# Kernel tuning notes

Hardware: AMD Instinct MI355X
Metric: run time of the kernel (lower is better)

Reference implementation:

```python
import jax, jax.numpy as jnp
import numpy as np

EPS = 1e-5  # torch LayerNorm default

def layer_norm(x, g, b):
    m = jnp.mean(x)
    v = jnp.mean((x - m) ** 2)  # biased variance, as in torch LayerNorm
    return (x - m) * jax.lax.rsqrt(v + EPS) * g + b

def setup_inputs() -> dict:
    key = jax.random.key(0)
    ks = jax.random.split(key, 8)
    sz_I, sz_H1, sz_H2, sz_O = 2048, 4096, 4096, 1024
    def w(k, out_d, in_d):
        return jax.random.normal(k, (out_d, in_d), dtype=jnp.float32) / np.sqrt(in_d)
    return {
        "input_raw": jax.random.normal(ks[0], (sz_I,), dtype=jnp.float32),
        "h2_prev": jax.random.normal(ks[1], (sz_H2,), dtype=jnp.float32),
        "W_I_H1": w(ks[2], sz_H1, sz_I),
        "W_H2_H1": w(ks[3], sz_H1, sz_H2),
        "W_H1_H2": w(ks[4], sz_H2, sz_H1),
        "W_H1_O": w(ks[5], sz_O, sz_H1),
        "W_H2_O": w(ks[6], sz_O, sz_H2),
        "g_H1": jnp.ones((sz_H1,), jnp.float32), "b_H1": jnp.zeros((sz_H1,), jnp.float32),
        "g_H2": jnp.ones((sz_H2,), jnp.float32), "b_H2": jnp.zeros((sz_H2,), jnp.float32),
        "g_O": jnp.ones((sz_O,), jnp.float32), "b_O": jnp.zeros((sz_O,), jnp.float32),
    }

def reference(input_raw, h2_prev, W_I_H1, W_H2_H1, W_H1_H2, W_H1_O, W_H2_O,
              g_H1, b_H1, g_H2, b_H2, g_O, b_O):
    act = jnp.tanh
    # message: out_act(in_act(LN_target(W @ x))); with tanh/identity composed = tanh once
    def msg(W, x, g, b):
        return act(layer_norm(W @ x, g, b))
    i_out = input_raw                                   # I layer output
    h1 = msg(W_I_H1, i_out, g_H1, b_H1) + msg(W_H2_H1, h2_prev, g_H1, b_H1)
    h2 = msg(W_H1_H2, h1, g_H2, b_H2)
    o_acc = msg(W_H1_O, h1, g_O, b_O) + msg(W_H2_O, h2, g_O, b_O)
    # final output-layer activation: out_act(LN_O(acc))
    o_final = act(layer_norm(o_acc, g_O, b_O))
    return o_final
```

## Files before the change

kernel.cpp:

```cpp
#include <hip/hip_runtime.h>

#define LN_EPS 1e-5f

__device__ __forceinline__ float wave_sum(float v) {
    #pragma unroll
    for (int o = 32; o; o >>= 1) v += __shfl_down(v, o);
    return v;
}

__device__ __forceinline__ float block_sum_1024(float v, float* sh) {
    int lane = threadIdx.x & 63, w = threadIdx.x >> 6;
    v = wave_sum(v);
    if (lane == 0) sh[w] = v;
    __syncthreads();
    if (w == 0) {
        float s = (lane < 16) ? sh[lane] : 0.f;
        #pragma unroll
        for (int o = 8; o; o >>= 1) s += __shfl_down(s, o);
        if (lane == 0) sh[0] = s;
    }
    __syncthreads();
    float r = sh[0];
    __syncthreads();
    return r;
}

__global__ __launch_bounds__(256) void k1(
        const float* __restrict__ W_I_H1, const float* __restrict__ x_in,
        const float* __restrict__ W_H2_H1, const float* __restrict__ h2_prev,
        float* __restrict__ t1, float* __restrict__ t2,
        float2* __restrict__ p1, float2* __restrict__ p2) {
    extern __shared__ float xs[];
    __shared__ float shy[4];
    const float* W; const float* x; float* y; float2* p; int C; int blk;
    if ((int)blockIdx.x < 1024) {
        W = W_I_H1;  x = x_in;    y = t1; p = p1; C = 2048; blk = blockIdx.x;
    } else {
        W = W_H2_H1; x = h2_prev; y = t2; p = p2; C = 4096; blk = blockIdx.x - 1024;
    }
    int n4 = C >> 2;
    float4* xs4 = (float4*)xs;
    for (int i = threadIdx.x; i < n4; i += 256)
        xs4[i] = ((const float4*)x)[i];
    __syncthreads();

    int wave = threadIdx.x >> 6, lane = threadIdx.x & 63;
    int row = blk * 4 + wave;
    const float4* Wr = (const float4*)(W + (size_t)row * C);
    float acc = 0.f;
    #pragma unroll 4
    for (int i = lane; i < n4; i += 64) {
        float4 w = Wr[i], v = xs4[i];
        acc += w.x * v.x + w.y * v.y + w.z * v.z + w.w * v.w;
    }
    acc = wave_sum(acc);
    if (lane == 0) { y[row] = acc; shy[wave] = acc; }
    __syncthreads();
    if (threadIdx.x == 0) {
        float s = 0.f, q = 0.f;
        #pragma unroll
        for (int i = 0; i < 4; i++) { float v = shy[i]; s += v; q += v * v; }
        p[blk] = make_float2(s, q);
    }
}

__global__ __launch_bounds__(1024) void ln2_add(
        const float* __restrict__ t1, const float* __restrict__ t2,
        const float2* __restrict__ p1, const float2* __restrict__ p2,
        const float* __restrict__ g, const float* __restrict__ b,
        float* __restrict__ h1) {
    __shared__ float sh[16];
    int tid = threadIdx.x;
    float2 a = p1[tid], c = p2[tid];
    float s1 = block_sum_1024(a.x, sh), q1 = block_sum_1024(a.y, sh);
    float s2 = block_sum_1024(c.x, sh), q2 = block_sum_1024(c.y, sh);
    const float invN = 1.f / 4096.f;
    float m1 = s1 * invN, r1 = rsqrtf(fmaxf(q1 * invN - m1 * m1, 0.f) + LN_EPS);
    float m2 = s2 * invN, r2 = rsqrtf(fmaxf(q2 * invN - m2 * m2, 0.f) + LN_EPS);

    float4 av = ((const float4*)t1)[tid], cv = ((const float4*)t2)[tid];
    float4 gv = ((const float4*)g)[tid], bv = ((const float4*)b)[tid];
    float4 o;
    o.x = tanhf((av.x - m1) * r1 * gv.x + bv.x) + tanhf((cv.x - m2) * r2 * gv.x + bv.x);
    o.y = tanhf((av.y - m1) * r1 * gv.y + bv.y) + tanhf((cv.y - m2) * r2 * gv.y + bv.y);
    o.z = tanhf((av.z - m1) * r1 * gv.z + bv.z) + tanhf((cv.z - m2) * r2 * gv.z + bv.z);
    o.w = tanhf((av.w - m1) * r1 * gv.w + bv.w) + tanhf((cv.w - m2) * r2 * gv.w + bv.w);
    ((float4*)h1)[tid] = o;
}

__global__ __launch_bounds__(256) void k2(
        const float* __restrict__ h1,
        const float* __restrict__ W_H1_H2, const float* __restrict__ W_H1_O,
        float* __restrict__ t3, float* __restrict__ t4,
        float2* __restrict__ p3, float2* __restrict__ p4) {
    extern __shared__ float xs[];
    __shared__ float shy[4];
    float4* xs4 = (float4*)xs;
    for (int i = threadIdx.x; i < 1024; i += 256)
        xs4[i] = ((const float4*)h1)[i];
    __syncthreads();

    const float* W; float* y; float2* p; int blk;
    if ((int)blockIdx.x < 1024) { W = W_H1_H2; y = t3; p = p3; blk = blockIdx.x; }
    else                        { W = W_H1_O;  y = t4; p = p4; blk = blockIdx.x - 1024; }
    int wave = threadIdx.x >> 6, lane = threadIdx.x & 63;
    int row = blk * 4 + wave;
    const float4* Wr = (const float4*)(W + (size_t)row * 4096);
    float acc = 0.f;
    #pragma unroll 4
    for (int i = lane; i < 1024; i += 64) {
        float4 w = Wr[i], v = xs4[i];
        acc += w.x * v.x + w.y * v.y + w.z * v.z + w.w * v.w;
    }
    acc = wave_sum(acc);
    if (lane == 0) { y[row] = acc; shy[wave] = acc; }
    __syncthreads();
    if (threadIdx.x == 0) {
        float s = 0.f, q = 0.f;
        #pragma unroll
        for (int i = 0; i < 4; i++) { float v = shy[i]; s += v; q += v * v; }
        p[blk] = make_float2(s, q);
    }
}

__global__ __launch_bounds__(1024) void ln_tanh(
        const float* __restrict__ t3, const float2* __restrict__ p3,
        const float* __restrict__ g, const float* __restrict__ b,
        float* __restrict__ h2) {
    __shared__ float sh[16];
    int tid = threadIdx.x;
    float2 a = p3[tid];
    float s3 = block_sum_1024(a.x, sh), q3 = block_sum_1024(a.y, sh);
    const float invN = 1.f / 4096.f;
    float m3 = s3 * invN, r3 = rsqrtf(fmaxf(q3 * invN - m3 * m3, 0.f) + LN_EPS);

    float4 av = ((const float4*)t3)[tid];
    float4 gv = ((const float4*)g)[tid], bv = ((const float4*)b)[tid];
    float4 o;
    o.x = tanhf((av.x - m3) * r3 * gv.x + bv.x);
    o.y = tanhf((av.y - m3) * r3 * gv.y + bv.y);
    o.z = tanhf((av.z - m3) * r3 * gv.z + bv.z);
    o.w = tanhf((av.w - m3) * r3 * gv.w + bv.w);
    ((float4*)h2)[tid] = o;
}

__global__ __launch_bounds__(256) void k3(
        const float* __restrict__ h2, const float* __restrict__ W_H2_O,
        float* __restrict__ t5, float2* __restrict__ p5) {
    extern __shared__ float xs[];
    __shared__ float shp[4];
    float4* xs4 = (float4*)xs;
    for (int i = threadIdx.x; i < 1024; i += 256)
        xs4[i] = ((const float4*)h2)[i];
    __syncthreads();

    int wave = threadIdx.x >> 6, lane = threadIdx.x & 63;
    int row  = blockIdx.x * 2 + (wave >> 1);
    int half = wave & 1;
    const float4* Wr = (const float4*)(W_H2_O + (size_t)row * 4096);
    float acc = 0.f;
    int i0 = half * 512 + lane;
    #pragma unroll 8
    for (int k = 0; k < 8; k++) {
        int i = i0 + k * 64;
        float4 w = Wr[i], v = xs4[i];
        acc += w.x * v.x + w.y * v.y + w.z * v.z + w.w * v.w;
    }
    acc = wave_sum(acc);
    if (lane == 0) shp[wave] = acc;
    __syncthreads();
    if (threadIdx.x == 0) {
        float r0 = shp[0] + shp[1], r1 = shp[2] + shp[3];
        t5[blockIdx.x * 2]     = r0;
        t5[blockIdx.x * 2 + 1] = r1;
        p5[blockIdx.x] = make_float2(r0 + r1, r0 * r0 + r1 * r1);
    }
}

__global__ __launch_bounds__(1024) void k4(
        const float* __restrict__ t4, const float* __restrict__ t5,
        const float2* __restrict__ p4, const float2* __restrict__ p5,
        const float* __restrict__ g, const float* __restrict__ b,
        float* __restrict__ out) {
    __shared__ float sh[16];
    int tid = threadIdx.x;
    float a4 = 0.f, c4 = 0.f, a5 = 0.f, c5 = 0.f;
    if (tid < 256) { float2 v = p4[tid]; a4 = v.x; c4 = v.y; }
    if (tid < 512) { float2 w = p5[tid]; a5 = w.x; c5 = w.y; }
    float s4 = block_sum_1024(a4, sh), q4 = block_sum_1024(c4, sh);
    float s5 = block_sum_1024(a5, sh), q5 = block_sum_1024(c5, sh);
    const float invN = 1.f / 1024.f;
    float m4 = s4 * invN, r4 = rsqrtf(fmaxf(q4 * invN - m4 * m4, 0.f) + LN_EPS);
    float m5 = s5 * invN, r5 = rsqrtf(fmaxf(q5 * invN - m5 * m5, 0.f) + LN_EPS);

    float gi = g[tid], bi = b[tid];
    float o = tanhf((t4[tid] - m4) * r4 * gi + bi)
            + tanhf((t5[tid] - m5) * r5 * gi + bi);

    float s = block_sum_1024(o, sh), q = block_sum_1024(o * o, sh);
    float m = s * invN, r = rsqrtf(fmaxf(q * invN - m * m, 0.f) + LN_EPS);
    out[tid] = tanhf((o - m) * r * gi + bi);
}

extern "C" void kernel_launch(void* const* d_in, const int* in_sizes, int n_in,
                              void* d_out, int out_size, void* d_ws, size_t ws_size,
                              hipStream_t stream) {
    const float* input_raw = (const float*)d_in[0];
    const float* h2_prev   = (const float*)d_in[1];
    const float* W_I_H1    = (const float*)d_in[2];
    const float* W_H2_H1   = (const float*)d_in[3];
    const float* W_H1_H2   = (const float*)d_in[4];
    const float* W_H1_O    = (const float*)d_in[5];
    const float* W_H2_O    = (const float*)d_in[6];
    const float* g_H1 = (const float*)d_in[7],  *b_H1 = (const float*)d_in[8];
    const float* g_H2 = (const float*)d_in[9],  *b_H2 = (const float*)d_in[10];
    const float* g_O  = (const float*)d_in[11], *b_O  = (const float*)d_in[12];
    float* out = (float*)d_out;

    float* ws = (float*)d_ws;
    float*  t1 = ws;
    float*  t2 = ws + 4096;
    float*  t3 = ws + 8192;
    float*  t4 = ws + 12288;
    float*  t5 = ws + 13312;
    float*  h1 = ws + 14336;
    float*  h2 = ws + 18432;
    float2* p1 = (float2*)(ws + 22528);
    float2* p2 = (float2*)(ws + 24576);
    float2* p3 = (float2*)(ws + 26624);
    float2* p4 = (float2*)(ws + 28672);
    float2* p5 = (float2*)(ws + 29184);

    const size_t lds = 4096 * sizeof(float);

    k1<<<2048, 256, lds, stream>>>(W_I_H1, input_raw, W_H2_H1, h2_prev,
                                   t1, t2, p1, p2);
    ln2_add<<<1, 1024, 0, stream>>>(t1, t2, p1, p2, g_H1, b_H1, h1);
    k2<<<1280, 256, lds, stream>>>(h1, W_H1_H2, W_H1_O, t3, t4, p3, p4);
    ln_tanh<<<1, 1024, 0, stream>>>(t3, p3, g_H2, b_H2, h2);
    k3<<<512, 256, lds, stream>>>(h2, W_H2_O, t5, p5);
    k4<<<1, 1024, 0, stream>>>(t4, t5, p4, p5, g_O, b_O, out);
}
```

Before: 237.5 us.

## Process two rows per wave in GEMVs and fuse paired block reductions

```diff
diff --git a/kernel.cpp b/kernel.cpp
--- a/kernel.cpp
+++ b/kernel.cpp
@@ -8,59 +8,87 @@
     return v;
 }
 
-__device__ __forceinline__ float block_sum_1024(float v, float* sh) {
+__device__ __forceinline__ float2 block_sum2_1024(float2 v, float2* sh) {
     int lane = threadIdx.x & 63, w = threadIdx.x >> 6;
-    v = wave_sum(v);
+    #pragma unroll
+    for (int o = 32; o; o >>= 1) {
+        v.x += __shfl_down(v.x, o);
+        v.y += __shfl_down(v.y, o);
+    }
     if (lane == 0) sh[w] = v;
     __syncthreads();
     if (w == 0) {
-        float s = (lane < 16) ? sh[lane] : 0.f;
+        float2 s = (lane < 16) ? sh[lane] : make_float2(0.f, 0.f);
         #pragma unroll
-        for (int o = 8; o; o >>= 1) s += __shfl_down(s, o);
+        for (int o = 8; o; o >>= 1) {
+            s.x += __shfl_down(s.x, o);
+            s.y += __shfl_down(s.y, o);
+        }
         if (lane == 0) sh[0] = s;
     }
     __syncthreads();
-    float r = sh[0];
+    float2 r = sh[0];
     __syncthreads();
     return r;
 }
 
-__global__ __launch_bounds__(256) void k1(
+__device__ __forceinline__ void stage_x(const float* __restrict__ x, int n4,
+                                        float4* __restrict__ xs4) {
+    for (int i = threadIdx.x; i < n4; i += 256)
+        xs4[i] = ((const float4*)x)[i];
+    __syncthreads();
+}
+
+template<int STEPS>
+__device__ __forceinline__ void gemv8(const float* __restrict__ W, int blk,
+                                      const float4* __restrict__ xs4,
+                                      float* __restrict__ y,
+                                      float2* __restrict__ p, bool want_p,
+                                      float* __restrict__ shy) {
+    const int C = STEPS * 256;
+    int wave = threadIdx.x >> 6, lane = threadIdx.x & 63;
+    int r0 = blk * 8 + wave * 2;
+    const float4* W0 = (const float4*)(W + (size_t)r0 * C);
+    const float4* W1 = (const float4*)(W + (size_t)(r0 + 1) * C);
+    float a00 = 0.f, a01 = 0.f, a10 = 0.f, a11 = 0.f;
+    #pragma unroll
+    for (int k = 0; k < STEPS; k++) {
+        int i = lane + (k << 6);
+        float4 w0 = W0[i], w1 = W1[i], v = xs4[i];
+        a00 += w0.x * v.x + w0.y * v.y;
+        a01 += w0.z * v.z + w0.w * v.w;
+        a10 += w1.x * v.x + w1.y * v.y;
+        a11 += w1.z * v.z + w1.w * v.w;
+    }
+    float v0 = wave_sum(a00 + a01);
+    float v1 = wave_sum(a10 + a11);
+    if (lane == 0) {
+        y[r0] = v0; y[r0 + 1] = v1;
+        shy[wave * 2] = v0; shy[wave * 2 + 1] = v1;
+    }
+    __syncthreads();
+    if (want_p && threadIdx.x == 0) {
+        float s = 0.f, q = 0.f;
+        #pragma unroll
+        for (int i = 0; i < 8; i++) { float t = shy[i]; s += t; q += t * t; }
+        p[blk] = make_float2(s, q);
+    }
+}
+
+__global__ __launch_bounds__(256, 4) void gA(
         const float* __restrict__ W_I_H1, const float* __restrict__ x_in,
         const float* __restrict__ W_H2_H1, const float* __restrict__ h2_prev,
         float* __restrict__ t1, float* __restrict__ t2,
         float2* __restrict__ p1, float2* __restrict__ p2) {
     extern __shared__ float xs[];
-    __shared__ float shy[4];
-    const float* W; const float* x; float* y; float2* p; int C; int blk;
-    if ((int)blockIdx.x < 1024) {
-        W = W_I_H1;  x = x_in;    y = t1; p = p1; C = 2048; blk = blockIdx.x;
+    __shared__ float shy[8];
+    float4* xs4 = (float4*)xs;
+    if ((int)blockIdx.x < 512) {
+        stage_x(x_in, 512, xs4);
+        gemv8<8>(W_I_H1, blockIdx.x, xs4, t1, p1, true, shy);
     } else {
-        W = W_H2_H1; x = h2_prev; y = t2; p = p2; C = 4096; blk = blockIdx.x - 1024;
-    }
-    int n4 = C >> 2;
-    float4* xs4 = (float4*)xs;
-    for (int i = threadIdx.x; i < n4; i += 256)
-        xs4[i] = ((const float4*)x)[i];
-    __syncthreads();
-
-    int wave = threadIdx.x >> 6, lane = threadIdx.x & 63;
-    int row = blk * 4 + wave;
-    const float4* Wr = (const float4*)(W + (size_t)row * C);
-    float acc = 0.f;
-    #pragma unroll 4
-    for (int i = lane; i < n4; i += 64) {
-        float4 w = Wr[i], v = xs4[i];
-        acc += w.x * v.x + w.y * v.y + w.z * v.z + w.w * v.w;
-    }
-    acc = wave_sum(acc);
-    if (lane == 0) { y[row] = acc; shy[wave] = acc; }
-    __syncthreads();
-    if (threadIdx.x == 0) {
-        float s = 0.f, q = 0.f;
-        #pragma unroll
-        for (int i = 0; i < 4; i++) { float v = shy[i]; s += v; q += v * v; }
-        p[blk] = make_float2(s, q);
+        stage_x(h2_prev, 1024, xs4);
+        gemv8<16>(W_H2_H1, blockIdx.x - 512, xs4, t2, p2, true, shy);
     }
 }
 
@@ -69,14 +97,15 @@
         const float2* __restrict__ p1, const float2* __restrict__ p2,
         const float* __restrict__ g, const float* __restrict__ b,
         float* __restrict__ h1) {
-    __shared__ float sh[16];
+    __shared__ float2 sh[16];
     int tid = threadIdx.x;
-    float2 a = p1[tid], c = p2[tid];
-    float s1 = block_sum_1024(a.x, sh), q1 = block_sum_1024(a.y, sh);
-    float s2 = block_sum_1024(c.x, sh), q2 = block_sum_1024(c.y, sh);
+    float2 a = (tid < 512) ? p1[tid] : make_float2(0.f, 0.f);
+    float2 c = (tid < 512) ? p2[tid] : make_float2(0.f, 0.f);
+    float2 S1 = block_sum2_1024(a, sh);
+    float2 S2 = block_sum2_1024(c, sh);
     const float invN = 1.f / 4096.f;
-    float m1 = s1 * invN, r1 = rsqrtf(fmaxf(q1 * invN - m1 * m1, 0.f) + LN_EPS);
-    float m2 = s2 * invN, r2 = rsqrtf(fmaxf(q2 * invN - m2 * m2, 0.f) + LN_EPS);
+    float m1 = S1.x * invN, r1 = rsqrtf(fmaxf(S1.y * invN - m1 * m1, 0.f) + LN_EPS);
+    float m2 = S2.x * invN, r2 = rsqrtf(fmaxf(S2.y * invN - m2 * m2, 0.f) + LN_EPS);
 
     float4 av = ((const float4*)t1)[tid], cv = ((const float4*)t2)[tid];
     float4 gv = ((const float4*)g)[tid], bv = ((const float4*)b)[tid];
@@ -88,38 +117,19 @@
     ((float4*)h1)[tid] = o;
 }
 
-__global__ __launch_bounds__(256) void k2(
+__global__ __launch_bounds__(256, 4) void gB(
         const float* __restrict__ h1,
         const float* __restrict__ W_H1_H2, const float* __restrict__ W_H1_O,
         float* __restrict__ t3, float* __restrict__ t4,
-        float2* __restrict__ p3, float2* __restrict__ p4) {
+        float2* __restrict__ p3) {
     extern __shared__ float xs[];
-    __shared__ float shy[4];
+    __shared__ float shy[8];
     float4* xs4 = (float4*)xs;
-    for (int i = threadIdx.x; i < 1024; i += 256)
-        xs4[i] = ((const float4*)h1)[i];
-    __syncthreads();
-
-    const float* W; float* y; float2* p; int blk;
-    if ((int)blockIdx.x < 1024) { W = W_H1_H2; y = t3; p = p3; blk = blockIdx.x; }
-    else                        { W = W_H1_O;  y = t4; p = p4; blk = blockIdx.x - 1024; }
-    int wave = threadIdx.x >> 6, lane = threadIdx.x & 63;
-    int row = blk * 4 + wave;
-    const float4* Wr = (const float4*)(W + (size_t)row * 4096);
-    float acc = 0.f;
-    #pragma unroll 4
-    for (int i = lane; i < 1024; i += 64) {
-        float4 w = Wr[i], v = xs4[i];
-        acc += w.x * v.x + w.y * v.y + w.z * v.z + w.w * v.w;
-    }
-    acc = wave_sum(acc);
-    if (lane == 0) { y[row] = acc; shy[wave] = acc; }
-    __syncthreads();
-    if (threadIdx.x == 0) {
-        float s = 0.f, q = 0.f;
-        #pragma unroll
-        for (int i = 0; i < 4; i++) { float v = shy[i]; s += v; q += v * v; }
-        p[blk] = make_float2(s, q);
+    stage_x(h1, 1024, xs4);
+    if ((int)blockIdx.x < 512) {
+        gemv8<16>(W_H1_H2, blockIdx.x, xs4, t3, p3, true, shy);
+    } else {
+        gemv8<16>(W_H1_O, blockIdx.x - 512, xs4, t4, (float2*)nullptr, false, shy);
     }
 }
 
@@ -127,12 +137,12 @@
         const float* __restrict__ t3, const float2* __restrict__ p3,
         const float* __restrict__ g, const float* __restrict__ b,
         float* __restrict__ h2) {
-    __shared__ float sh[16];
+    __shared__ float2 sh[16];
     int tid = threadIdx.x;
-    float2 a = p3[tid];
-    float s3 = block_sum_1024(a.x, sh), q3 = block_sum_1024(a.y, sh);
+    float2 a = (tid < 512) ? p3[tid] : make_float2(0.f, 0.f);
+    float2 S3 = block_sum2_1024(a, sh);
     const float invN = 1.f / 4096.f;
-    float m3 = s3 * invN, r3 = rsqrtf(fmaxf(q3 * invN - m3 * m3, 0.f) + LN_EPS);
+    float m3 = S3.x * invN, r3 = rsqrtf(fmaxf(S3.y * invN - m3 * m3, 0.f) + LN_EPS);
 
     float4 av = ((const float4*)t3)[tid];
     float4 gv = ((const float4*)g)[tid], bv = ((const float4*)b)[tid];
@@ -144,61 +154,45 @@
     ((float4*)h2)[tid] = o;
 }
 
-__global__ __launch_bounds__(256) void k3(
+__global__ __launch_bounds__(256, 4) void gC(
         const float* __restrict__ h2, const float* __restrict__ W_H2_O,
-        float* __restrict__ t5, float2* __restrict__ p5) {
+        float* __restrict__ t5) {
     extern __shared__ float xs[];
-    __shared__ float shp[4];
     float4* xs4 = (float4*)xs;
-    for (int i = threadIdx.x; i < 1024; i += 256)
-        xs4[i] = ((const float4*)h2)[i];
-    __syncthreads();
-
+    stage_x(h2, 1024, xs4);
     int wave = threadIdx.x >> 6, lane = threadIdx.x & 63;
-    int row  = blockIdx.x * 2 + (wave >> 1);
-    int half = wave & 1;
+    int row = blockIdx.x * 4 + wave;
     const float4* Wr = (const float4*)(W_H2_O + (size_t)row * 4096);
-    float acc = 0.f;
-    int i0 = half * 512 + lane;
-    #pragma unroll 8
-    for (int k = 0; k < 8; k++) {
-        int i = i0 + k * 64;
+    float a0 = 0.f, a1 = 0.f, a2 = 0.f, a3 = 0.f;
+    #pragma unroll
+    for (int k = 0; k < 16; k++) {
+        int i = lane + (k << 6);
         float4 w = Wr[i], v = xs4[i];
-        acc += w.x * v.x + w.y * v.y + w.z * v.z + w.w * v.w;
-    }
-    acc = wave_sum(acc);
-    if (lane == 0) shp[wave] = acc;
-    __syncthreads();
-    if (threadIdx.x == 0) {
-        float r0 = shp[0] + shp[1], r1 = shp[2] + shp[3];
-        t5[blockIdx.x * 2]     = r0;
-        t5[blockIdx.x * 2 + 1] = r1;
-        p5[blockIdx.x] = make_float2(r0 + r1, r0 * r0 + r1 * r1);
-    }
+        a0 += w.x * v.x; a1 += w.y * v.y; a2 += w.z * v.z; a3 += w.w * v.w;
+    }
+    float r = wave_sum((a0 + a1) + (a2 + a3));
+    if (lane == 0) t5[row] = r;
 }
 
 __global__ __launch_bounds__(1024) void k4(
         const float* __restrict__ t4, const float* __restrict__ t5,
-        const float2* __restrict__ p4, const float2* __restrict__ p5,
         const float* __restrict__ g, const float* __restrict__ b,
         float* __restrict__ out) {
-    __shared__ float sh[16];
+    __shared__ float2 sh[16];
     int tid = threadIdx.x;
-    float a4 = 0.f, c4 = 0.f, a5 = 0.f, c5 = 0.f;
-    if (tid < 256) { float2 v = p4[tid]; a4 = v.x; c4 = v.y; }
-    if (tid < 512) { float2 w = p5[tid]; a5 = w.x; c5 = w.y; }
-    float s4 = block_sum_1024(a4, sh), q4 = block_sum_1024(c4, sh);
-    float s5 = block_sum_1024(a5, sh), q5 = block_sum_1024(c5, sh);
     const float invN = 1.f / 1024.f;
-    float m4 = s4 * invN, r4 = rsqrtf(fmaxf(q4 * invN - m4 * m4, 0.f) + LN_EPS);
-    float m5 = s5 * invN, r5 = rsqrtf(fmaxf(q5 * invN - m5 * m5, 0.f) + LN_EPS);
+    float x4 = t4[tid], x5 = t5[tid];
+    float2 S4 = block_sum2_1024(make_float2(x4, x4 * x4), sh);
+    float2 S5 = block_sum2_1024(make_float2(x5, x5 * x5), sh);
+    float m4 = S4.x * invN, r4 = rsqrtf(fmaxf(S4.y * invN - m4 * m4, 0.f) + LN_EPS);
+    float m5 = S5.x * invN, r5 = rsqrtf(fmaxf(S5.y * invN - m5 * m5, 0.f) + LN_EPS);
 
     float gi = g[tid], bi = b[tid];
-    float o = tanhf((t4[tid] - m4) * r4 * gi + bi)
-            + tanhf((t5[tid] - m5) * r5 * gi + bi);
-
-    float s = block_sum_1024(o, sh), q = block_sum_1024(o * o, sh);
-    float m = s * invN, r = rsqrtf(fmaxf(q * invN - m * m, 0.f) + LN_EPS);
+    float o = tanhf((x4 - m4) * r4 * gi + bi)
+            + tanhf((x5 - m5) * r5 * gi + bi);
+
+    float2 SO = block_sum2_1024(make_float2(o, o * o), sh);
+    float m = SO.x * invN, r = rsqrtf(fmaxf(SO.y * invN - m * m, 0.f) + LN_EPS);
     out[tid] = tanhf((o - m) * r * gi + bi);
 }
 
@@ -226,18 +220,16 @@
     float*  h1 = ws + 14336;
     float*  h2 = ws + 18432;
     float2* p1 = (float2*)(ws + 22528);
-    float2* p2 = (float2*)(ws + 24576);
-    float2* p3 = (float2*)(ws + 26624);
-    float2* p4 = (float2*)(ws + 28672);
-    float2* p5 = (float2*)(ws + 29184);
+    float2* p2 = (float2*)(ws + 23552);
+    float2* p3 = (float2*)(ws + 24576);
 
     const size_t lds = 4096 * sizeof(float);
 
-    k1<<<2048, 256, lds, stream>>>(W_I_H1, input_raw, W_H2_H1, h2_prev,
+    gA<<<1024, 256, lds, stream>>>(W_I_H1, input_raw, W_H2_H1, h2_prev,
                                    t1, t2, p1, p2);
     ln2_add<<<1, 1024, 0, stream>>>(t1, t2, p1, p2, g_H1, b_H1, h1);
-    k2<<<1280, 256, lds, stream>>>(h1, W_H1_H2, W_H1_O, t3, t4, p3, p4);
+    gB<<<640, 256, lds, stream>>>(h1, W_H1_H2, W_H1_O, t3, t4, p3);
     ln_tanh<<<1, 1024, 0, stream>>>(t3, p3, g_H2, b_H2, h2);
-    k3<<<512, 256, lds, stream>>>(h2, W_H2_O, t5, p5);
-    k4<<<1, 1024, 0, stream>>>(t4, t5, p4, p5, g_O, b_O, out);
-}
+    gC<<<256, 256, lds, stream>>>(h2, W_H2_O, t5);
+    k4<<<1, 1024, 0, stream>>>(t4, t5, g_O, b_O, out);
+}
```

After: 233.7 us (median of 2 runs). About the same (-1.6%).
